# Kernel tuning notes

Hardware: AMD Instinct MI355X
Metric: run time of the kernel (lower is better)

## Reference

```python
import jax, jax.numpy as jnp
import numpy as np
from jax import lax

B, C, H, W = 16, 256, 128, 128
MAX_ROOMS = 10

def _conv(x, w, b):
    y = lax.conv_general_dilated(x, w, window_strides=(1, 1), padding='SAME',
                                 dimension_numbers=('NCHW', 'OIHW', 'NCHW'))
    return y + b[None, :, None, None]

def setup_inputs() -> dict:
    key = jax.random.key(0)
    ks = jax.random.split(key, 16)
    def w(k, shape, fan_in):
        return jax.random.normal(k, shape, jnp.float32) * (1.0 / np.sqrt(fan_in))
    inp = {
        'features': jax.random.normal(ks[0], (B, C, H, W), jnp.float32),
        'conv1_w': w(ks[1], (C // 2, C, 3, 3), C * 9),
        'conv1_b': jnp.zeros((C // 2,), jnp.float32),
        'conv2_w': w(ks[2], (MAX_ROOMS, C // 2, 3, 3), (C // 2) * 9),
        'conv2_b': jnp.zeros((MAX_ROOMS,), jnp.float32),
        'lin1_w': w(ks[3], (256, C * 64), C * 64),
        'lin1_b': jnp.zeros((256,), jnp.float32),
        'lin2_w': w(ks[4], (128, 256), 256),
        'lin2_b': jnp.zeros((128,), jnp.float32),
        'adj1_w': w(ks[5], (64, 256), 256),
        'adj1_b': jnp.zeros((64,), jnp.float32),
        'adj2_w': w(ks[6], (32, 64), 64),
        'adj2_b': jnp.zeros((32,), jnp.float32),
        'adj3_w': w(ks[7], (1, 32), 32),
        'adj3_b': jnp.zeros((1,), jnp.float32),
    }
    return inp

def reference(features, conv1_w, conv1_b, conv2_w, conv2_b,
              lin1_w, lin1_b, lin2_w, lin2_b,
              adj1_w, adj1_b, adj2_w, adj2_b, adj3_w, adj3_b):
    # room detector: conv -> relu -> conv -> sigmoid
    h = jax.nn.relu(_conv(features, conv1_w, conv1_b))
    room_maps = jax.nn.sigmoid(_conv(h, conv2_w, conv2_b))  # [B, max_rooms, H, W]

    # room features: adaptive avg pool to 8x8 (exact since H,W divisible by 8)
    b, c = features.shape[0], features.shape[1]
    pooled = features.reshape(b, c, 8, H // 8, 8, W // 8).mean(axis=(3, 5))  # [B,C,8,8]
    flat = pooled.reshape(b, c * 64)
    feat = jax.nn.relu(flat @ lin1_w.T + lin1_b) @ lin2_w.T + lin2_b  # [B,128]

    # adjacency: original loop uses the SAME pair_feat=cat([feat,feat]) for every (i,j),
    # so compute one prob per batch row and broadcast to all off-diagonal entries.
    pair = jnp.concatenate([feat, feat], axis=-1)  # [B,256]
    a = jax.nn.relu(pair @ adj1_w.T + adj1_b)
    a = jax.nn.relu(a @ adj2_w.T + adj2_b)
    p = jax.nn.sigmoid(a @ adj3_w.T + adj3_b)  # [B,1]
    off_diag = 1.0 - jnp.eye(MAX_ROOMS, dtype=features.dtype)
    adjacency = p[:, :, None] * off_diag[None]  # [B, max_rooms, max_rooms]

    return room_maps, feat, adjacency
```

## Files before the change

kernel.cpp:

```cpp
#include <hip/hip_runtime.h>

#define HH 128
#define WW 128
#define FEAT_OFF 2621440ull
#define ADJ_OFF  2623488ull

typedef __bf16 bf16x8 __attribute__((ext_vector_type(8)));
typedef float  f32x4  __attribute__((ext_vector_type(4)));

__device__ __forceinline__ unsigned short f2bf(float f) {
  unsigned int u = __float_as_uint(f);
  unsigned int r = ((u >> 16) & 1u) + 0x7fffu;
  return (unsigned short)((u + r) >> 16);
}
__device__ __forceinline__ void gl_lds16(const void* g, void* l) {
  __builtin_amdgcn_global_load_lds((const __attribute__((address_space(1))) unsigned int*)g,
                                   (__attribute__((address_space(3))) unsigned int*)l, 16, 0, 0);
}
__device__ __forceinline__ int SW(int r) { return (r ^ (r >> 2)) & 3; }

#define FENCE() asm volatile("" ::: "memory")
#define BARRIER() do { FENCE(); __builtin_amdgcn_s_barrier(); FENCE(); } while (0)
#define LBAR() do { asm volatile("s_waitcnt lgkmcnt(0)" ::: "memory"); __builtin_amdgcn_s_barrier(); FENCE(); } while (0)

__global__ void prep_kernel(const float* __restrict__ w1, const float* __restrict__ w2,
                            unsigned short* __restrict__ W1t, unsigned short* __restrict__ W2t,
                            unsigned short* __restrict__ zp) {
  int id = blockIdx.x * 256 + threadIdx.x;
  if (id < 2048) zp[id] = 0;
  if (id < 294912) {
    int ci = id & 255, co = (id >> 8) & 127, dxy = id >> 15;
    int dy = dxy / 3, dx = dxy - 3 * dy;
    W1t[id] = f2bf(w1[((co * 256 + ci) * 3 + dy) * 3 + dx]);
  }
  if (id < 18432) {
    int ci = id & 127, co = (id >> 7) & 15, dxy = id >> 11;
    int dy = dxy / 3, dx = dxy - 3 * dy;
    W2t[id] = (co < 10) ? f2bf(w2[((co * 128 + ci) * 3 + dy) * 3 + dx]) : (unsigned short)0;
  }
}

__global__ void nhwc_kernel(const float* __restrict__ F, unsigned short* __restrict__ Xn) {
  __shared__ __align__(16) unsigned short tile[16384];
  int t = threadIdx.x, bi = blockIdx.x;
  int chalf = bi & 1, y = (bi >> 1) & 127, b = bi >> 8;
  int c0 = chalf * 128;
  int cp = t >> 2, xq = t & 3;
  const float* rowA = F + (((size_t)(b * 256 + c0 + cp * 2)) * HH + y) * WW + xq * 32;
  const float* rowB = rowA + (size_t)HH * WW;
  unsigned int* tw = (unsigned int*)tile;
#pragma unroll
  for (int jj = 0; jj < 8; ++jj) {
    float4 va = *(const float4*)(rowA + jj * 4);
    float4 vb = *(const float4*)(rowB + jj * 4);
    float av[4] = {va.x, va.y, va.z, va.w};
    float bv[4] = {vb.x, vb.y, vb.z, vb.w};
#pragma unroll
    for (int e = 0; e < 4; ++e) {
      int x = xq * 32 + jj * 4 + e;
      unsigned int word = (unsigned int)f2bf(av[e]) | ((unsigned int)f2bf(bv[e]) << 16);
      tw[x * 64 + (((cp >> 2) ^ (x & 15)) << 2) + (cp & 3)] = word;
    }
  }
  __syncthreads();
  int x = t >> 1, h = t & 1;
  unsigned short* dst = Xn + ((((size_t)b * HH + y) * WW) + x) * 256 + c0;
#pragma unroll
  for (int k = 0; k < 8; ++k) {
    int s = h * 8 + k;
    *(uint4*)(dst + s * 8) = *(const uint4*)(tile + x * 128 + ((s ^ (x & 15)) << 3));
  }
}

__global__ __launch_bounds__(512, 2) void conv1_kernel(const unsigned short* __restrict__ X,
                                                       const unsigned short* __restrict__ Wt,
                                                       const float* __restrict__ bias,
                                                       unsigned short* __restrict__ Hout,
                                                       const unsigned short* __restrict__ zp) {
  extern __shared__ __align__(16) unsigned short smem[];
  const int t = threadIdx.x, l = t & 63, w = t >> 6;
  int bid = (blockIdx.x & 7) * 64 + (blockIdx.x >> 3);
  const int b = bid >> 5, y0 = (bid & 31) * 4;
  const int ko = l >> 4, r0 = l & 15;
  const int yloc = w >> 1, xh = w & 1, xoff = xh * 64;

  f32x4 acc[4][8];
#pragma unroll
  for (int i = 0; i < 4; ++i)
#pragma unroll
    for (int j = 0; j < 8; ++j) acc[i][j] = {0.f, 0.f, 0.f, 0.f};

  auto stage = [&](int p, int bufsel) {
    int dy = p >> 3, cb = p & 7;
    unsigned short* buf = smem + bufsel * 30720;
    for (int c = w; c < 60; c += 8) {
      const unsigned short* g;
      if (c < 36) {
        int air = c / 9, jj = c - air * 9;
        int er = jj * 16 + (l >> 2);
        int xin = er - 1;
        int row = y0 - 1 + dy + air;
        if (row >= 0 && row < HH && xin >= 0 && xin < WW && er < 130) {
          int kq = (l & 3) ^ SW(er);
          g = X + (((size_t)b * HH + row) * WW + xin) * 256 + cb * 32 + kq * 8;
        } else g = zp + l * 8;
      } else {
        int cc = c - 36;
        int dxi = cc >> 3, jj = cc & 7;
        int co = jj * 16 + (l >> 2);
        int kq = (l & 3) ^ SW(co);
        g = Wt + (((size_t)(dy * 3 + dxi)) * 128 + co) * 256 + cb * 32 + kq * 8;
      }
      gl_lds16(g, buf + c * 512);
    }
  };

  stage(0, 0);
  for (int p = 0; p < 24; ++p) {
    if (p < 23) {
      stage(p + 1, (p + 1) & 1);
      FENCE();
      asm volatile("s_waitcnt vmcnt(7)" ::: "memory");
    } else {
      FENCE();
      asm volatile("s_waitcnt vmcnt(0)" ::: "memory");
    }
    BARRIER();
    const unsigned short* buf = smem + (p & 1) * 30720;
    const unsigned short* Ab = buf + yloc * 4608;
    const unsigned short* Bb = buf + 18432;
#pragma unroll
    for (int dx = 0; dx < 3; ++dx) {
      bf16x8 a[4], bb[8];
#pragma unroll
      for (int mf = 0; mf < 4; ++mf) {
        int er = xoff + mf * 16 + r0 + dx;
        a[mf] = *(const bf16x8*)(Ab + er * 32 + ((ko ^ SW(er)) << 3));
      }
#pragma unroll
      for (int nf = 0; nf < 8; ++nf) {
        int co = nf * 16 + r0;
        bb[nf] = *(const bf16x8*)(Bb + dx * 4096 + co * 32 + ((ko ^ SW(co)) << 3));
      }
#pragma unroll
      for (int mf = 0; mf < 4; ++mf)
#pragma unroll
        for (int nf = 0; nf < 8; ++nf)
          acc[mf][nf] = __builtin_amdgcn_mfma_f32_16x16x32_bf16(a[mf], bb[nf], acc[mf][nf], 0, 0, 0);
    }
    BARRIER();
  }

  unsigned short* E = smem;
  for (int r = 0; r < 2; ++r) {
    if (xh == r) {
#pragma unroll
      for (int nf = 0; nf < 8; ++nf) {
        int co = nf * 16 + r0;
        float bv = bias[co];
#pragma unroll
        for (int mf = 0; mf < 4; ++mf)
#pragma unroll
          for (int j = 0; j < 4; ++j) {
            int xl = mf * 16 + ko * 4 + j;
            E[yloc * 8192 + xl * 128 + co] = f2bf(fmaxf(acc[mf][nf][j] + bv, 0.f));
          }
      }
    }
    LBAR();
#pragma unroll
    for (int k = 0; k < 8; ++k) {
      int idx = k * 512 + t;
      int yl = idx >> 10, rem = idx & 1023;
      int xl = rem >> 4, oct = rem & 15;
      size_t g = (((size_t)b * HH + y0 + yl) * WW + r * 64 + xl) * 128 + oct * 8;
      *(uint4*)(Hout + g) = ((const uint4*)E)[idx];
    }
    LBAR();
  }
}

__global__ __launch_bounds__(256) void conv2_kernel(const unsigned short* __restrict__ Hn,
                                                    const unsigned short* __restrict__ Wt,
                                                    const float* __restrict__ bias,
                                                    float* __restrict__ rmaps,
                                                    const unsigned short* __restrict__ zp) {
  extern __shared__ __align__(16) unsigned short smem[];
  const int t = threadIdx.x, l = t & 63, w = t >> 6;
  int bid = (blockIdx.x & 7) * 64 + (blockIdx.x >> 3);
  const int b = bid >> 5, y0 = (bid & 31) * 4;
  const int ko = l >> 4, r0 = l & 15;
  const int yloc = w;

  f32x4 acc[8];
#pragma unroll
  for (int i = 0; i < 8; ++i) acc[i] = {0.f, 0.f, 0.f, 0.f};

  auto stage = [&](int cb, int bufsel) {
    unsigned short* buf = smem + bufsel * 32256;
    for (int c = w; c < 63; c += 4) {
      const unsigned short* g;
      if (c < 54) {
        int air = c / 9, jj = c - air * 9;
        int er = jj * 16 + (l >> 2);
        int xin = er - 1;
        int row = y0 - 1 + air;
        if (row >= 0 && row < HH && xin >= 0 && xin < WW && er < 130) {
          int kq = (l & 3) ^ SW(er);
          g = Hn + (((size_t)b * HH + row) * WW + xin) * 128 + cb * 32 + kq * 8;
        } else g = zp + l * 8;
      } else {
        int tap = c - 54;
        int co = l >> 2;
        int kq = (l & 3) ^ SW(co);
        g = Wt + ((size_t)tap * 16 + co) * 128 + cb * 32 + kq * 8;
      }
      gl_lds16(g, buf + c * 512);
    }
  };

  stage(0, 0);
  for (int p = 0; p < 4; ++p) {
    if (p < 3) {
      stage(p + 1, (p + 1) & 1);
      FENCE();
      asm volatile("s_waitcnt vmcnt(15)" ::: "memory");
    } else {
      FENCE();
      asm volatile("s_waitcnt vmcnt(0)" ::: "memory");
    }
    BARRIER();
    const unsigned short* buf = smem + (p & 1) * 32256;
#pragma unroll
    for (int dy = 0; dy < 3; ++dy) {
      const unsigned short* Ab = buf + (yloc + dy) * 4608;
#pragma unroll
      for (int dx = 0; dx < 3; ++dx) {
        int tap = dy * 3 + dx;
        bf16x8 bbf = *(const bf16x8*)(buf + (54 + tap) * 512 + r0 * 32 + ((ko ^ SW(r0)) << 3));
#pragma unroll
        for (int mf = 0; mf < 8; ++mf) {
          int er = mf * 16 + r0 + dx;
          bf16x8 a = *(const bf16x8*)(Ab + er * 32 + ((ko ^ SW(er)) << 3));
          acc[mf] = __builtin_amdgcn_mfma_f32_16x16x32_bf16(a, bbf, acc[mf], 0, 0, 0);
        }
      }
    }
    BARRIER();
  }

  int co = r0;
  if (co < 10) {
    float bv = bias[co];
    int y = y0 + yloc;
#pragma unroll
    for (int mf = 0; mf < 8; ++mf) {
      int x = mf * 16 + ko * 4;
      float4 o;
      o.x = 1.f / (1.f + __expf(-(acc[mf][0] + bv)));
      o.y = 1.f / (1.f + __expf(-(acc[mf][1] + bv)));
      o.z = 1.f / (1.f + __expf(-(acc[mf][2] + bv)));
      o.w = 1.f / (1.f + __expf(-(acc[mf][3] + bv)));
      *(float4*)&rmaps[(((size_t)b * 10 + co) * HH + y) * WW + x] = o;
    }
  }
}

__global__ void pool2_kernel(const unsigned short* __restrict__ Xn, float* __restrict__ pooled) {
  int t = threadIdx.x, bi = blockIdx.x;
  int b = bi >> 6, py = (bi >> 3) & 7, px = bi & 7;
  int p = t & 127, half = t >> 7;
  float s0 = 0.f, s1 = 0.f;
  const unsigned short* base = Xn + (((size_t)b * HH + py * 16 + half * 8) * WW + px * 16) * 256 + p * 2;
  for (int i = 0; i < 8; ++i)
#pragma unroll
    for (int j = 0; j < 16; ++j) {
      unsigned int v = *(const unsigned int*)(base + ((size_t)i * WW + j) * 256);
      s0 += __uint_as_float(v << 16);
      s1 += __uint_as_float(v & 0xffff0000u);
    }
  __shared__ float red[2][256];
  red[half][p * 2] = s0;
  red[half][p * 2 + 1] = s1;
  __syncthreads();
  float v = red[0][t] + red[1][t];
  pooled[(size_t)b * 16384 + t * 64 + py * 8 + px] = v * (1.f / 256.f);
}

__global__ void lin1_kernel(const float* __restrict__ pooled, const float* __restrict__ w1,
                            const float* __restrict__ b1, float* __restrict__ hidden) {
  int o = blockIdx.x, t = threadIdx.x;
  float acc[16];
#pragma unroll
  for (int b = 0; b < 16; ++b) acc[b] = 0.f;
  const float* wr = w1 + (size_t)o * 16384;
  for (int i = t; i < 16384; i += 256) {
    float wv = wr[i];
#pragma unroll
    for (int b = 0; b < 16; ++b) acc[b] += wv * pooled[(size_t)b * 16384 + i];
  }
  __shared__ float red[16][4];
#pragma unroll
  for (int b = 0; b < 16; ++b) {
    float v = acc[b];
    for (int s = 32; s; s >>= 1) v += __shfl_down(v, s);
    if ((t & 63) == 0) red[b][t >> 6] = v;
  }
  __syncthreads();
  if (t < 16) {
    float v = red[t][0] + red[t][1] + red[t][2] + red[t][3] + b1[o];
    hidden[o * 16 + t] = fmaxf(v, 0.f);
  }
}

__global__ void head_kernel(const float* __restrict__ hidden,
                            const float* __restrict__ w2, const float* __restrict__ b2,
                            const float* __restrict__ a1w, const float* __restrict__ a1b,
                            const float* __restrict__ a2w, const float* __restrict__ a2b,
                            const float* __restrict__ a3w, const float* __restrict__ a3b,
                            float* __restrict__ out) {
  int b = blockIdx.x, t = threadIdx.x;
  __shared__ float hid[256], fs[128], a1[64], a2[32], pv;
  hid[t] = hidden[t * 16 + b];
  __syncthreads();
  if (t < 128) {
    float s = b2[t];
    for (int k = 0; k < 256; ++k) s += hid[k] * w2[t * 256 + k];
    fs[t] = s;
    out[FEAT_OFF + b * 128 + t] = s;
  }
  __syncthreads();
  if (t < 64) {
    float s = a1b[t];
    for (int k = 0; k < 128; ++k) s += fs[k] * (a1w[t * 256 + k] + a1w[t * 256 + 128 + k]);
    a1[t] = fmaxf(s, 0.f);
  }
  __syncthreads();
  if (t < 32) {
    float s = a2b[t];
    for (int k = 0; k < 64; ++k) s += a1[k] * a2w[t * 64 + k];
    a2[t] = fmaxf(s, 0.f);
  }
  __syncthreads();
  if (t == 0) {
    float s = a3b[0];
    for (int k = 0; k < 32; ++k) s += a2[k] * a3w[k];
    pv = 1.f / (1.f + __expf(-s));
  }
  __syncthreads();
  if (t < 100) out[ADJ_OFF + b * 100 + t] = ((t / 10) == (t % 10)) ? 0.f : pv;
}

extern "C" void kernel_launch(void* const* d_in, const int* in_sizes, int n_in,
                              void* d_out, int out_size, void* d_ws, size_t ws_size,
                              hipStream_t stream) {
  const float* F   = (const float*)d_in[0];
  const float* w1  = (const float*)d_in[1];
  const float* b1  = (const float*)d_in[2];
  const float* w2  = (const float*)d_in[3];
  const float* b2  = (const float*)d_in[4];
  const float* l1w = (const float*)d_in[5];
  const float* l1b = (const float*)d_in[6];
  const float* l2w = (const float*)d_in[7];
  const float* l2b = (const float*)d_in[8];
  const float* a1w = (const float*)d_in[9];
  const float* a1b = (const float*)d_in[10];
  const float* a2w = (const float*)d_in[11];
  const float* a2b = (const float*)d_in[12];
  const float* a3w = (const float*)d_in[13];
  const float* a3b = (const float*)d_in[14];
  float* out = (float*)d_out;
  char* ws = (char*)d_ws;

  const size_t zp_off   = 0;
  const size_t w1t_off  = 4096;
  const size_t w2t_off  = w1t_off + 589824;
  const size_t xn_off   = w2t_off + 36864;
  const size_t hn_off   = xn_off + 134217728ull;
  const size_t pool_off = hn_off + 67108864ull;
  const size_t hid_off  = pool_off + 1048576ull;
  const size_t need     = hid_off + 16384ull;
  if (ws_size < need) return;

  unsigned short* zp  = (unsigned short*)(ws + zp_off);
  unsigned short* W1t = (unsigned short*)(ws + w1t_off);
  unsigned short* W2t = (unsigned short*)(ws + w2t_off);
  unsigned short* Xn  = (unsigned short*)(ws + xn_off);
  unsigned short* Hn  = (unsigned short*)(ws + hn_off);
  float* pooled = (float*)(ws + pool_off);
  float* hidden = (float*)(ws + hid_off);

  hipFuncSetAttribute((const void*)conv1_kernel, hipFuncAttributeMaxDynamicSharedMemorySize, 122880);
  hipFuncSetAttribute((const void*)conv2_kernel, hipFuncAttributeMaxDynamicSharedMemorySize, 129024);

  prep_kernel<<<1152, 256, 0, stream>>>(w1, w2, W1t, W2t, zp);
  nhwc_kernel<<<4096, 256, 0, stream>>>(F, Xn);
  pool2_kernel<<<1024, 256, 0, stream>>>(Xn, pooled);
  conv1_kernel<<<512, 512, 122880, stream>>>(Xn, W1t, b1, Hn, zp);
  conv2_kernel<<<512, 256, 129024, stream>>>(Hn, W2t, b2, out, zp);
  lin1_kernel<<<256, 256, 0, stream>>>(pooled, l1w, l1b, hidden);
  head_kernel<<<16, 256, 0, stream>>>(hidden, l2w, l2b, a1w, a1b, a2w, a2b, a3w, a3b, out);
}
```

Measured before the change: 379.6 us.

## Fuse avg-pool partial sums into NHWC transpose and widen conv1 per-wave tiles

The NHWC conversion kernel now also computes per-row, per-16-column partial sums in fp32. A small pool3 kernel reduces those partials, which replaces the pool2 pass that re-read the whole bf16 NHWC tensor. Separately, conv1 drops from 512 to 256 threads per block. Each wave now covers a full 128-wide row with 8x8 MFMA accumulators, which doubles register pressure and cuts occupancy to one block per CU. The epilogue gets a padded LDS layout, and the partials buffer reuses the Hn workspace before conv1 overwrites it.

```diff
diff --git a/kernel.cpp b/kernel.cpp
--- a/kernel.cpp
+++ b/kernel.cpp
@@ -40,8 +40,10 @@
   }
 }
 
-__global__ void nhwc_kernel(const float* __restrict__ F, unsigned short* __restrict__ Xn) {
+__global__ void nhwc_kernel(const float* __restrict__ F, unsigned short* __restrict__ Xn,
+                            float* __restrict__ part) {
   __shared__ __align__(16) unsigned short tile[16384];
+  __shared__ float pl[1024];
   int t = threadIdx.x, bi = blockIdx.x;
   int chalf = bi & 1, y = (bi >> 1) & 127, b = bi >> 8;
   int c0 = chalf * 128;
@@ -49,6 +51,7 @@
   const float* rowA = F + (((size_t)(b * 256 + c0 + cp * 2)) * HH + y) * WW + xq * 32;
   const float* rowB = rowA + (size_t)HH * WW;
   unsigned int* tw = (unsigned int*)tile;
+  float s00 = 0.f, s01 = 0.f, s10 = 0.f, s11 = 0.f;
 #pragma unroll
   for (int jj = 0; jj < 8; ++jj) {
     float4 va = *(const float4*)(rowA + jj * 4);
@@ -57,11 +60,17 @@
     float bv[4] = {vb.x, vb.y, vb.z, vb.w};
 #pragma unroll
     for (int e = 0; e < 4; ++e) {
-      int x = xq * 32 + jj * 4 + e;
+      int xl = jj * 4 + e;
+      int x = xq * 32 + xl;
+      if (xl < 16) { s00 += av[e]; s10 += bv[e]; } else { s01 += av[e]; s11 += bv[e]; }
       unsigned int word = (unsigned int)f2bf(av[e]) | ((unsigned int)f2bf(bv[e]) << 16);
       tw[x * 64 + (((cp >> 2) ^ (x & 15)) << 2) + (cp & 3)] = word;
     }
   }
+  pl[(cp * 2 + 0) * 8 + xq * 2 + 0] = s00;
+  pl[(cp * 2 + 0) * 8 + xq * 2 + 1] = s01;
+  pl[(cp * 2 + 1) * 8 + xq * 2 + 0] = s10;
+  pl[(cp * 2 + 1) * 8 + xq * 2 + 1] = s11;
   __syncthreads();
   int x = t >> 1, h = t & 1;
   unsigned short* dst = Xn + ((((size_t)b * HH + y) * WW) + x) * 256 + c0;
@@ -70,9 +79,25 @@
     int s = h * 8 + k;
     *(uint4*)(dst + s * 8) = *(const uint4*)(tile + x * 128 + ((s ^ (x & 15)) << 3));
   }
-}
-
-__global__ __launch_bounds__(512, 2) void conv1_kernel(const unsigned short* __restrict__ X,
+  *(float4*)&part[((((size_t)b * 128 + y) * 2) + chalf) * 1024 + t * 4] = *(const float4*)&pl[t * 4];
+}
+
+__global__ void pool3_kernel(const float* __restrict__ part, float* __restrict__ pooled) {
+  int bi = blockIdx.x, t = threadIdx.x;
+  int py = bi & 7, chalf = (bi >> 3) & 1, b = bi >> 4;
+#pragma unroll
+  for (int q = 0; q < 4; ++q) {
+    int i = q * 256 + t;
+    float s = 0.f;
+#pragma unroll
+    for (int yy = 0; yy < 16; ++yy)
+      s += part[((((size_t)b * 128 + py * 16 + yy) * 2) + chalf) * 1024 + i];
+    int ch = i >> 3, px = i & 7;
+    pooled[(size_t)b * 16384 + (chalf * 128 + ch) * 64 + py * 8 + px] = s * (1.f / 256.f);
+  }
+}
+
+__global__ __launch_bounds__(256, 1) void conv1_kernel(const unsigned short* __restrict__ X,
                                                        const unsigned short* __restrict__ Wt,
                                                        const float* __restrict__ bias,
                                                        unsigned short* __restrict__ Hout,
@@ -82,18 +107,17 @@
   int bid = (blockIdx.x & 7) * 64 + (blockIdx.x >> 3);
   const int b = bid >> 5, y0 = (bid & 31) * 4;
   const int ko = l >> 4, r0 = l & 15;
-  const int yloc = w >> 1, xh = w & 1, xoff = xh * 64;
-
-  f32x4 acc[4][8];
-#pragma unroll
-  for (int i = 0; i < 4; ++i)
+
+  f32x4 acc[8][8];
+#pragma unroll
+  for (int i = 0; i < 8; ++i)
 #pragma unroll
     for (int j = 0; j < 8; ++j) acc[i][j] = {0.f, 0.f, 0.f, 0.f};
 
   auto stage = [&](int p, int bufsel) {
     int dy = p >> 3, cb = p & 7;
     unsigned short* buf = smem + bufsel * 30720;
-    for (int c = w; c < 60; c += 8) {
+    for (int c = w; c < 60; c += 4) {
       const unsigned short* g;
       if (c < 36) {
         int air = c / 9, jj = c - air * 9;
@@ -120,21 +144,21 @@
     if (p < 23) {
       stage(p + 1, (p + 1) & 1);
       FENCE();
-      asm volatile("s_waitcnt vmcnt(7)" ::: "memory");
+      asm volatile("s_waitcnt vmcnt(15)" ::: "memory");
     } else {
       FENCE();
       asm volatile("s_waitcnt vmcnt(0)" ::: "memory");
     }
     BARRIER();
     const unsigned short* buf = smem + (p & 1) * 30720;
-    const unsigned short* Ab = buf + yloc * 4608;
+    const unsigned short* Ab = buf + w * 4608;
     const unsigned short* Bb = buf + 18432;
 #pragma unroll
     for (int dx = 0; dx < 3; ++dx) {
-      bf16x8 a[4], bb[8];
-#pragma unroll
-      for (int mf = 0; mf < 4; ++mf) {
-        int er = xoff + mf * 16 + r0 + dx;
+      bf16x8 a[8], bb[8];
+#pragma unroll
+      for (int mf = 0; mf < 8; ++mf) {
+        int er = mf * 16 + r0 + dx;
         a[mf] = *(const bf16x8*)(Ab + er * 32 + ((ko ^ SW(er)) << 3));
       }
 #pragma unroll
@@ -143,7 +167,7 @@
         bb[nf] = *(const bf16x8*)(Bb + dx * 4096 + co * 32 + ((ko ^ SW(co)) << 3));
       }
 #pragma unroll
-      for (int mf = 0; mf < 4; ++mf)
+      for (int mf = 0; mf < 8; ++mf)
 #pragma unroll
         for (int nf = 0; nf < 8; ++nf)
           acc[mf][nf] = __builtin_amdgcn_mfma_f32_16x16x32_bf16(a[mf], bb[nf], acc[mf][nf], 0, 0, 0);
@@ -153,28 +177,29 @@
 
   unsigned short* E = smem;
   for (int r = 0; r < 2; ++r) {
-    if (xh == r) {
+    if ((w >> 1) == r) {
+      int half = w & 1;
 #pragma unroll
       for (int nf = 0; nf < 8; ++nf) {
         int co = nf * 16 + r0;
         float bv = bias[co];
 #pragma unroll
-        for (int mf = 0; mf < 4; ++mf)
+        for (int mf = 0; mf < 8; ++mf)
 #pragma unroll
           for (int j = 0; j < 4; ++j) {
-            int xl = mf * 16 + ko * 4 + j;
-            E[yloc * 8192 + xl * 128 + co] = f2bf(fmaxf(acc[mf][nf][j] + bv, 0.f));
+            int x = mf * 16 + ko * 4 + j;
+            E[half * 17408 + x * 136 + co] = f2bf(fmaxf(acc[mf][nf][j] + bv, 0.f));
           }
       }
     }
     LBAR();
 #pragma unroll
-    for (int k = 0; k < 8; ++k) {
-      int idx = k * 512 + t;
-      int yl = idx >> 10, rem = idx & 1023;
-      int xl = rem >> 4, oct = rem & 15;
-      size_t g = (((size_t)b * HH + y0 + yl) * WW + r * 64 + xl) * 128 + oct * 8;
-      *(uint4*)(Hout + g) = ((const uint4*)E)[idx];
+    for (int k = 0; k < 16; ++k) {
+      int idx = k * 256 + t;
+      int yl = idx >> 11, x = (idx >> 4) & 127, cc = idx & 15;
+      const uint4 v = *(const uint4*)(E + yl * 17408 + x * 136 + cc * 8);
+      size_t g = (((size_t)b * HH + y0 + r * 2 + yl) * WW + x) * 128 + cc * 8;
+      *(uint4*)(Hout + g) = v;
     }
     LBAR();
   }
@@ -264,27 +289,6 @@
       *(float4*)&rmaps[(((size_t)b * 10 + co) * HH + y) * WW + x] = o;
     }
   }
-}
-
-__global__ void pool2_kernel(const unsigned short* __restrict__ Xn, float* __restrict__ pooled) {
-  int t = threadIdx.x, bi = blockIdx.x;
-  int b = bi >> 6, py = (bi >> 3) & 7, px = bi & 7;
-  int p = t & 127, half = t >> 7;
-  float s0 = 0.f, s1 = 0.f;
-  const unsigned short* base = Xn + (((size_t)b * HH + py * 16 + half * 8) * WW + px * 16) * 256 + p * 2;
-  for (int i = 0; i < 8; ++i)
-#pragma unroll
-    for (int j = 0; j < 16; ++j) {
-      unsigned int v = *(const unsigned int*)(base + ((size_t)i * WW + j) * 256);
-      s0 += __uint_as_float(v << 16);
-      s1 += __uint_as_float(v & 0xffff0000u);
-    }
-  __shared__ float red[2][256];
-  red[half][p * 2] = s0;
-  red[half][p * 2 + 1] = s1;
-  __syncthreads();
-  float v = red[0][t] + red[1][t];
-  pooled[(size_t)b * 16384 + t * 64 + py * 8 + px] = v * (1.f / 256.f);
 }
 
 __global__ void lin1_kernel(const float* __restrict__ pooled, const float* __restrict__ w1,
@@ -387,6 +391,7 @@
   unsigned short* W2t = (unsigned short*)(ws + w2t_off);
   unsigned short* Xn  = (unsigned short*)(ws + xn_off);
   unsigned short* Hn  = (unsigned short*)(ws + hn_off);
+  float* part   = (float*)(ws + hn_off);
   float* pooled = (float*)(ws + pool_off);
   float* hidden = (float*)(ws + hid_off);
 
@@ -394,9 +399,9 @@
   hipFuncSetAttribute((const void*)conv2_kernel, hipFuncAttributeMaxDynamicSharedMemorySize, 129024);
 
   prep_kernel<<<1152, 256, 0, stream>>>(w1, w2, W1t, W2t, zp);
-  nhwc_kernel<<<4096, 256, 0, stream>>>(F, Xn);
-  pool2_kernel<<<1024, 256, 0, stream>>>(Xn, pooled);
-  conv1_kernel<<<512, 512, 122880, stream>>>(Xn, W1t, b1, Hn, zp);
+  nhwc_kernel<<<4096, 256, 0, stream>>>(F, Xn, part);
+  pool3_kernel<<<256, 256, 0, stream>>>(part, pooled);
+  conv1_kernel<<<512, 256, 122880, stream>>>(Xn, W1t, b1, Hn, zp);
   conv2_kernel<<<512, 256, 129024, stream>>>(Hn, W2t, b2, out, zp);
   lin1_kernel<<<256, 256, 0, stream>>>(pooled, l1w, l1b, hidden);
   head_kernel<<<16, 256, 0, stream>>>(hidden, l2w, l2b, a1w, a1b, a2w, a2b, a3w, a3b, out);
```

Measured after the change: 495.6 us. 1.31x slower.

## Fuse avg-pool partial sums into NHWC conversion and drop Xn re-read

Applied to the files above, without the earlier changes.

The NHWC/bf16 conversion kernel now also computes per-row 16-wide partial sums of the fp32 input. A small pool3 kernel reduces these over 16 rows into the pooled features, replacing pool2, which re-read the whole bf16 Xn tensor. The partial buffer reuses the Hn workspace region before conv1 writes it. The conversion kernel is also restructured to use fp32 LDS staging with more shared memory. conv1 loses its min-blocks launch hint.

```diff
diff --git a/kernel.cpp b/kernel.cpp
--- a/kernel.cpp
+++ b/kernel.cpp
@@ -40,43 +40,66 @@
   }
 }
 
-__global__ void nhwc_kernel(const float* __restrict__ F, unsigned short* __restrict__ Xn) {
-  __shared__ __align__(16) unsigned short tile[16384];
-  int t = threadIdx.x, bi = blockIdx.x;
-  int chalf = bi & 1, y = (bi >> 1) & 127, b = bi >> 8;
-  int c0 = chalf * 128;
-  int cp = t >> 2, xq = t & 3;
-  const float* rowA = F + (((size_t)(b * 256 + c0 + cp * 2)) * HH + y) * WW + xq * 32;
-  const float* rowB = rowA + (size_t)HH * WW;
-  unsigned int* tw = (unsigned int*)tile;
-#pragma unroll
-  for (int jj = 0; jj < 8; ++jj) {
-    float4 va = *(const float4*)(rowA + jj * 4);
-    float4 vb = *(const float4*)(rowB + jj * 4);
-    float av[4] = {va.x, va.y, va.z, va.w};
-    float bv[4] = {vb.x, vb.y, vb.z, vb.w};
-#pragma unroll
-    for (int e = 0; e < 4; ++e) {
-      int x = xq * 32 + jj * 4 + e;
-      unsigned int word = (unsigned int)f2bf(av[e]) | ((unsigned int)f2bf(bv[e]) << 16);
-      tw[x * 64 + (((cp >> 2) ^ (x & 15)) << 2) + (cp & 3)] = word;
-    }
-  }
-  __syncthreads();
-  int x = t >> 1, h = t & 1;
-  unsigned short* dst = Xn + ((((size_t)b * HH + y) * WW) + x) * 256 + c0;
-#pragma unroll
-  for (int k = 0; k < 8; ++k) {
-    int s = h * 8 + k;
-    *(uint4*)(dst + s * 8) = *(const uint4*)(tile + x * 128 + ((s ^ (x & 15)) << 3));
-  }
-}
-
-__global__ __launch_bounds__(512, 2) void conv1_kernel(const unsigned short* __restrict__ X,
-                                                       const unsigned short* __restrict__ Wt,
-                                                       const float* __restrict__ bias,
-                                                       unsigned short* __restrict__ Hout,
-                                                       const unsigned short* __restrict__ zp) {
+__global__ void nhwc_kernel(const float* __restrict__ F, unsigned short* __restrict__ Xn,
+                            float* __restrict__ part) {
+  extern __shared__ __align__(16) float smemf[];
+  float* ld = smemf;
+  float* pl = smemf + 128 * 132;
+  const int t = threadIdx.x, l = t & 63, w = t >> 6;
+  const int y = blockIdx.x & 127, b = blockIdx.x >> 7;
+
+  for (int r = 0; r < 2; ++r) {
+#pragma unroll
+    for (int i = 0; i < 16; ++i) {
+      int c = w * 32 + i * 2 + (l >> 5);
+      int x0 = (l & 31) * 4;
+      float4 v = *(const float4*)&F[(((size_t)(b * 256 + r * 128 + c)) * HH + y) * WW + x0];
+      float s = v.x + v.y + v.z + v.w;
+      s += __shfl_down(s, 1);
+      s += __shfl_down(s, 2);
+      if ((l & 3) == 0) pl[(r * 128 + c) * 8 + ((l & 31) >> 2)] = s;
+      *(float4*)&ld[c * 132 + x0] = v;
+    }
+    __syncthreads();
+    {
+      int x = t >> 1, h = t & 1;
+      unsigned short* dst = Xn + ((((size_t)b * HH + y) * WW) + x) * 256 + r * 128 + h * 64;
+#pragma unroll
+      for (int kk = 0; kk < 8; ++kk) {
+        __align__(16) unsigned short v[8];
+#pragma unroll
+        for (int j = 0; j < 8; ++j)
+          v[j] = f2bf(ld[(h * 64 + kk * 8 + j) * 132 + x]);
+        *(uint4*)(dst + kk * 8) = *(const uint4*)v;
+      }
+    }
+    __syncthreads();
+  }
+  float* pd = part + ((size_t)b * 128 + y) * 2048;
+  *(float4*)&pd[t * 8]     = *(const float4*)&pl[t * 8];
+  *(float4*)&pd[t * 8 + 4] = *(const float4*)&pl[t * 8 + 4];
+}
+
+__global__ void pool3_kernel(const float* __restrict__ part, float* __restrict__ pooled) {
+  int bi = blockIdx.x, t = threadIdx.x;
+  int py = bi & 7, b = bi >> 3;
+#pragma unroll
+  for (int q = 0; q < 8; ++q) {
+    int i = q * 256 + t;
+    float s = 0.f;
+#pragma unroll
+    for (int yy = 0; yy < 16; ++yy)
+      s += part[((size_t)b * 128 + py * 16 + yy) * 2048 + i];
+    int c = i >> 3, px = i & 7;
+    pooled[(size_t)b * 16384 + c * 64 + py * 8 + px] = s * (1.f / 256.f);
+  }
+}
+
+__global__ __launch_bounds__(512) void conv1_kernel(const unsigned short* __restrict__ X,
+                                                    const unsigned short* __restrict__ Wt,
+                                                    const float* __restrict__ bias,
+                                                    unsigned short* __restrict__ Hout,
+                                                    const unsigned short* __restrict__ zp) {
   extern __shared__ __align__(16) unsigned short smem[];
   const int t = threadIdx.x, l = t & 63, w = t >> 6;
   int bid = (blockIdx.x & 7) * 64 + (blockIdx.x >> 3);
@@ -266,27 +289,6 @@
   }
 }
 
-__global__ void pool2_kernel(const unsigned short* __restrict__ Xn, float* __restrict__ pooled) {
-  int t = threadIdx.x, bi = blockIdx.x;
-  int b = bi >> 6, py = (bi >> 3) & 7, px = bi & 7;
-  int p = t & 127, half = t >> 7;
-  float s0 = 0.f, s1 = 0.f;
-  const unsigned short* base = Xn + (((size_t)b * HH + py * 16 + half * 8) * WW + px * 16) * 256 + p * 2;
-  for (int i = 0; i < 8; ++i)
-#pragma unroll
-    for (int j = 0; j < 16; ++j) {
-      unsigned int v = *(const unsigned int*)(base + ((size_t)i * WW + j) * 256);
-      s0 += __uint_as_float(v << 16);
-      s1 += __uint_as_float(v & 0xffff0000u);
-    }
-  __shared__ float red[2][256];
-  red[half][p * 2] = s0;
-  red[half][p * 2 + 1] = s1;
-  __syncthreads();
-  float v = red[0][t] + red[1][t];
-  pooled[(size_t)b * 16384 + t * 64 + py * 8 + px] = v * (1.f / 256.f);
-}
-
 __global__ void lin1_kernel(const float* __restrict__ pooled, const float* __restrict__ w1,
                             const float* __restrict__ b1, float* __restrict__ hidden) {
   int o = blockIdx.x, t = threadIdx.x;
@@ -387,15 +389,17 @@
   unsigned short* W2t = (unsigned short*)(ws + w2t_off);
   unsigned short* Xn  = (unsigned short*)(ws + xn_off);
   unsigned short* Hn  = (unsigned short*)(ws + hn_off);
+  float* part   = (float*)(ws + hn_off);
   float* pooled = (float*)(ws + pool_off);
   float* hidden = (float*)(ws + hid_off);
 
+  hipFuncSetAttribute((const void*)nhwc_kernel,  hipFuncAttributeMaxDynamicSharedMemorySize, 75776);
   hipFuncSetAttribute((const void*)conv1_kernel, hipFuncAttributeMaxDynamicSharedMemorySize, 122880);
   hipFuncSetAttribute((const void*)conv2_kernel, hipFuncAttributeMaxDynamicSharedMemorySize, 129024);
 
   prep_kernel<<<1152, 256, 0, stream>>>(w1, w2, W1t, W2t, zp);
-  nhwc_kernel<<<4096, 256, 0, stream>>>(F, Xn);
-  pool2_kernel<<<1024, 256, 0, stream>>>(Xn, pooled);
+  nhwc_kernel<<<2048, 256, 75776, stream>>>(F, Xn, part);
+  pool3_kernel<<<128, 256, 0, stream>>>(part, pooled);
   conv1_kernel<<<512, 512, 122880, stream>>>(Xn, W1t, b1, Hn, zp);
   conv2_kernel<<<512, 256, 129024, stream>>>(Hn, W2t, b2, out, zp);
   lin1_kernel<<<256, 256, 0, stream>>>(pooled, l1w, l1b, hidden);
```

After: 416.0 us. 1.1x slower.
